# Kernel optimization log

Measured on AMD Instinct MI355X. Metric: run time of the kernel, lower is better.

The kernel has to match this reference:

```python
import jax, jax.numpy as jnp
import numpy as np

DIST_THRESHOLD = 0.1
CLIP_MAX = 0.2
VIOL_SCALE = 0.25

B, H, L, S, W = 16, 64, 12, 8, 256


def setup_inputs() -> dict:
    key = jax.random.key(0)
    k1, k2, k3, k4, k5, k6 = jax.random.split(key, 6)
    link_pos_seq = jax.random.normal(k1, (B, H, L, 3), dtype=jnp.float32)
    link_rot_seq = jax.random.normal(k2, (B, H, L, 3, 3), dtype=jnp.float32)
    # per-link robot collision spheres in link frame: [L, S, 4] (cx,cy,cz,r)
    rob_centers = 0.1 * jax.random.normal(k3, (L, S, 3), dtype=jnp.float32)
    rob_radii = 0.02 + 0.08 * jax.random.uniform(k4, (L, S, 1), dtype=jnp.float32)
    link_spheres = jnp.concatenate([rob_centers, rob_radii], axis=-1)
    # world obstacle spheres: [W, 4]
    w_centers = 2.0 * jax.random.normal(k5, (W, 3), dtype=jnp.float32)
    w_radii = 0.05 + 0.2 * jax.random.uniform(k6, (W, 1), dtype=jnp.float32)
    world_spheres = jnp.concatenate([w_centers, w_radii], axis=-1)
    weight = jnp.asarray(1.0, dtype=jnp.float32)
    return {"link_pos_seq": link_pos_seq, "link_rot_seq": link_rot_seq,
            "link_spheres": link_spheres, "world_spheres": world_spheres,
            "weight": weight}


def reference(link_pos_seq, link_rot_seq, link_spheres, world_spheres, weight):
    b, h, l, _ = link_pos_seq.shape
    n = b * h
    pos = link_pos_seq.reshape(n, l, 3)           # [N,L,3]
    rot = link_rot_seq.reshape(n, l, 3, 3)        # [N,L,3,3]
    # transform link-frame sphere centers into world frame
    centers = jnp.einsum('nlij,lsj->nlsi', rot, link_spheres[..., :3]) + pos[:, :, None, :]  # [N,L,S,3]
    rob_r = link_spheres[..., 3]                  # [L,S]
    w_c = world_spheres[:, :3]                    # [W,3]
    w_r = world_spheres[:, 3]                     # [W]
    # pairwise center distance robot-sphere vs world-sphere
    diff = centers[:, :, :, None, :] - w_c[None, None, None, :, :]   # [N,L,S,W,3]
    center_dist = jnp.sqrt(jnp.sum(diff * diff, axis=-1))            # [N,L,S,W]
    signed = w_r[None, None, None, :] - center_dist + rob_r[None, :, :, None]
    dist = jnp.max(jnp.max(signed, axis=-1), axis=-1)                # [N,L]
    dist = dist.reshape(b, h, l)
    # _shape_violation: shift, clip to [0, clip_max], scale, sum over links
    d = jnp.clip(dist + DIST_THRESHOLD, 0.0, CLIP_MAX) / VIOL_SCALE
    violation = jnp.sum(d, axis=-1)               # [B,H]
    cost = weight * violation
    return cost
```

## Files before the change

kernel.cpp:

```cpp
#include <hip/hip_runtime.h>


#define NL 12
#define NS 8

__device__ __forceinline__ float fast_sqrtf(float x) {
    return __builtin_amdgcn_sqrtf(x);
}

__global__ __launch_bounds__(256, 4) void pcc_kernel(
    const float* __restrict__ pos,
    const float* __restrict__ rot,
    const float* __restrict__ lsph,
    const float* __restrict__ wsph,
    const float* __restrict__ weight,
    float* __restrict__ out)
{
    const int n    = blockIdx.x;
    const int tid  = threadIdx.x;
    const int lane = tid & 63;
    const int wave = tid >> 6;

    __shared__ float4 cen[NL * NS];
    __shared__ float partial[4];

    if (tid < NL * NS) {
        const int l = tid >> 3;
        const float* r = rot + ((size_t)n * NL + l) * 9;
        const float* p = pos + ((size_t)n * NL + l) * 3;
        const float4 ls = reinterpret_cast<const float4*>(lsph)[tid];
        const float cx = r[0]*ls.x + r[1]*ls.y + r[2]*ls.z + p[0];
        const float cy = r[3]*ls.x + r[4]*ls.y + r[5]*ls.z + p[1];
        const float cz = r[6]*ls.x + r[7]*ls.y + r[8]*ls.z + p[2];
        cen[tid] = make_float4(cx, cy, cz, ls.w);
    }

    const float4* wsph4 = reinterpret_cast<const float4*>(wsph);
    const float4 ws0 = wsph4[lane];
    const float4 ws1 = wsph4[lane + 64];
    const float4 ws2 = wsph4[lane + 128];
    const float4 ws3 = wsph4[lane + 192];

    __syncthreads();

    float m[3];
    m[0] = m[1] = m[2] = -1e30f;
    const float4* base = &cen[wave * 24];

#pragma unroll
    for (int i = 0; i < 24; ++i) {
        const float4 c = base[i];
        const float rr = c.w;

        const float dx0 = c.x - ws0.x, dy0 = c.y - ws0.y, dz0 = c.z - ws0.z;
        const float dx1 = c.x - ws1.x, dy1 = c.y - ws1.y, dz1 = c.z - ws1.z;
        const float dx2 = c.x - ws2.x, dy2 = c.y - ws2.y, dz2 = c.z - ws2.z;
        const float dx3 = c.x - ws3.x, dy3 = c.y - ws3.y, dz3 = c.z - ws3.z;

        const float v0 = ws0.w + rr - fast_sqrtf(dx0*dx0 + dy0*dy0 + dz0*dz0);
        const float v1 = ws1.w + rr - fast_sqrtf(dx1*dx1 + dy1*dy1 + dz1*dz1);
        const float v2 = ws2.w + rr - fast_sqrtf(dx2*dx2 + dy2*dy2 + dz2*dz2);
        const float v3 = ws3.w + rr - fast_sqrtf(dx3*dx3 + dy3*dy3 + dz3*dz3);

        const int li = i >> 3;
        m[li] = fmaxf(fmaxf(m[li], v0), v1);
        m[li] = fmaxf(fmaxf(m[li], v2), v3);
    }

#pragma unroll
    for (int off = 1; off < 64; off <<= 1) {
        m[0] = fmaxf(m[0], __shfl_xor(m[0], off));
        m[1] = fmaxf(m[1], __shfl_xor(m[1], off));
        m[2] = fmaxf(m[2], __shfl_xor(m[2], off));
    }

    const float acc = fminf(fmaxf(m[0] + 0.1f, 0.0f), 0.2f) * 4.0f
                    + fminf(fmaxf(m[1] + 0.1f, 0.0f), 0.2f) * 4.0f
                    + fminf(fmaxf(m[2] + 0.1f, 0.0f), 0.2f) * 4.0f;

    if (lane == 0) partial[wave] = acc;
    __syncthreads();
    if (tid == 0)
        out[n] = weight[0] * (partial[0] + partial[1] + partial[2] + partial[3]);
}

extern "C" void kernel_launch(void* const* d_in, const int* in_sizes, int n_in,
                              void* d_out, int out_size, void* d_ws, size_t ws_size,
                              hipStream_t stream) {
    const float* pos    = (const float*)d_in[0];
    const float* rot    = (const float*)d_in[1];
    const float* lsph   = (const float*)d_in[2];
    const float* wsph   = (const float*)d_in[3];
    const float* weight = (const float*)d_in[4];
    float* out = (float*)d_out;

    const int N = out_size;
    pcc_kernel<<<N, 256, 0, stream>>>(pos, rot, lsph, wsph, weight, out);
}
```

Baseline: 13.50 us.

## Expand squared distance algebraically and compute with packed FP32 FMA

Rewrites the squared distance as |c|^2 + |w|^2 - 2c·w so each robot-sphere pair needs only one add and three FMAs. Pairs of world spheres are processed with v_pk_add_f32 and v_pk_fma_f32 inline asm, and the robot radius is added once after the max. Centres are stored duplicated into v2f pairs in shared memory, which doubles LDS traffic. The expansion can lose precision through cancellation, so the result is clamped at zero before the sqrt. The launch-bounds occupancy hint is also dropped.

```diff
diff --git a/kernel.cpp b/kernel.cpp
--- a/kernel.cpp
+++ b/kernel.cpp
@@ -4,11 +4,24 @@
 #define NL 12
 #define NS 8
 
+typedef float v2f __attribute__((ext_vector_type(2)));
+
 __device__ __forceinline__ float fast_sqrtf(float x) {
     return __builtin_amdgcn_sqrtf(x);
 }
 
-__global__ __launch_bounds__(256, 4) void pcc_kernel(
+__device__ __forceinline__ v2f pk_add(v2f a, v2f b) {
+    v2f d;
+    asm("v_pk_add_f32 %0, %1, %2" : "=v"(d) : "v"(a), "v"(b));
+    return d;
+}
+__device__ __forceinline__ void pk_fma(v2f& acc, v2f a, v2f b) {
+    asm("v_pk_fma_f32 %0, %1, %2, %0" : "+v"(acc) : "v"(a), "v"(b));
+}
+
+struct alignas(16) Cen { v2f cx, cy, cz, c2; };
+
+__global__ __launch_bounds__(256) void pcc_kernel(
     const float* __restrict__ pos,
     const float* __restrict__ rot,
     const float* __restrict__ lsph,
@@ -21,7 +34,8 @@
     const int lane = tid & 63;
     const int wave = tid >> 6;
 
-    __shared__ float4 cen[NL * NS];
+    __shared__ Cen   cdup[NL * NS];
+    __shared__ float rrs[NL * NS];
     __shared__ float partial[4];
 
     if (tid < NL * NS) {
@@ -32,7 +46,14 @@
         const float cx = r[0]*ls.x + r[1]*ls.y + r[2]*ls.z + p[0];
         const float cy = r[3]*ls.x + r[4]*ls.y + r[5]*ls.z + p[1];
         const float cz = r[6]*ls.x + r[7]*ls.y + r[8]*ls.z + p[2];
-        cen[tid] = make_float4(cx, cy, cz, ls.w);
+        const float c2 = cx*cx + cy*cy + cz*cz;
+        Cen c;
+        c.cx = (v2f){cx, cx};
+        c.cy = (v2f){cy, cy};
+        c.cz = (v2f){cz, cz};
+        c.c2 = (v2f){c2, c2};
+        cdup[tid] = c;
+        rrs[tid]  = ls.w;
     }
 
     const float4* wsph4 = reinterpret_cast<const float4*>(wsph);
@@ -40,31 +61,41 @@
     const float4 ws1 = wsph4[lane + 64];
     const float4 ws2 = wsph4[lane + 128];
     const float4 ws3 = wsph4[lane + 192];
+    const v2f nwxA = {-2.f*ws0.x, -2.f*ws1.x}, nwyA = {-2.f*ws0.y, -2.f*ws1.y}, nwzA = {-2.f*ws0.z, -2.f*ws1.z};
+    const v2f nwxB = {-2.f*ws2.x, -2.f*ws3.x}, nwyB = {-2.f*ws2.y, -2.f*ws3.y}, nwzB = {-2.f*ws2.z, -2.f*ws3.z};
+    const v2f qA = {ws0.x*ws0.x + ws0.y*ws0.y + ws0.z*ws0.z,
+                    ws1.x*ws1.x + ws1.y*ws1.y + ws1.z*ws1.z};
+    const v2f qB = {ws2.x*ws2.x + ws2.y*ws2.y + ws2.z*ws2.z,
+                    ws3.x*ws3.x + ws3.y*ws3.y + ws3.z*ws3.z};
+    const float wr0 = ws0.w, wr1 = ws1.w, wr2 = ws2.w, wr3 = ws3.w;
 
     __syncthreads();
 
     float m[3];
     m[0] = m[1] = m[2] = -1e30f;
-    const float4* base = &cen[wave * 24];
+    const Cen*   base  = &cdup[wave * 24];
+    const float* baser = &rrs[wave * 24];
 
 #pragma unroll
     for (int i = 0; i < 24; ++i) {
-        const float4 c = base[i];
-        const float rr = c.w;
+        const Cen c = base[i];
 
-        const float dx0 = c.x - ws0.x, dy0 = c.y - ws0.y, dz0 = c.z - ws0.z;
-        const float dx1 = c.x - ws1.x, dy1 = c.y - ws1.y, dz1 = c.z - ws1.z;
-        const float dx2 = c.x - ws2.x, dy2 = c.y - ws2.y, dz2 = c.z - ws2.z;
-        const float dx3 = c.x - ws3.x, dy3 = c.y - ws3.y, dz3 = c.z - ws3.z;
+        v2f dA = pk_add(qA, c.c2);
+        v2f dB = pk_add(qB, c.c2);
+        pk_fma(dA, c.cx, nwxA);
+        pk_fma(dB, c.cx, nwxB);
+        pk_fma(dA, c.cy, nwyA);
+        pk_fma(dB, c.cy, nwyB);
+        pk_fma(dA, c.cz, nwzA);
+        pk_fma(dB, c.cz, nwzB);
 
-        const float v0 = ws0.w + rr - fast_sqrtf(dx0*dx0 + dy0*dy0 + dz0*dz0);
-        const float v1 = ws1.w + rr - fast_sqrtf(dx1*dx1 + dy1*dy1 + dz1*dz1);
-        const float v2 = ws2.w + rr - fast_sqrtf(dx2*dx2 + dy2*dy2 + dz2*dz2);
-        const float v3 = ws3.w + rr - fast_sqrtf(dx3*dx3 + dy3*dy3 + dz3*dz3);
+        const float g0 = wr0 - fast_sqrtf(fmaxf(dA.x, 0.0f));
+        const float g1 = wr1 - fast_sqrtf(fmaxf(dA.y, 0.0f));
+        const float g2 = wr2 - fast_sqrtf(fmaxf(dB.x, 0.0f));
+        const float g3 = wr3 - fast_sqrtf(fmaxf(dB.y, 0.0f));
 
         const int li = i >> 3;
-        m[li] = fmaxf(fmaxf(m[li], v0), v1);
-        m[li] = fmaxf(fmaxf(m[li], v2), v3);
+        m[li] = fmaxf(m[li], fmaxf(fmaxf(g0, g1), fmaxf(g2, g3)) + baser[i]);
     }
 
 #pragma unroll
```

New measurement: 13.07 us. 3.2% less time.
